# Kernel tuning notes

Hardware: AMD Instinct MI355X
Metric: run time of the kernel (lower is better)

The kernel has to match this reference:

```python
import jax, jax.numpy as jnp
import numpy as np

SR = 16000
WIN_LENGTH = int(round(SR / 1000.0 * 25))   # 400 samples
HOP_LENGTH = int(round(SR / 1000.0 * 10))   # 160 samples
EPSILON = 1e-12


def _hamming_window(n):
    # torch.hamming_window(n, periodic=True): 0.54 - 0.46*cos(2*pi*k/n)
    k = jnp.arange(n, dtype=jnp.float32)
    return 0.54 - 0.46 * jnp.cos(2.0 * jnp.pi * k / n)


def _fit_window(win, n_fft):
    # Replicates the module's pad-to / crop-to n_fft logic (static shapes).
    L = win.shape[0]
    if L < n_fft:
        pad = n_fft - L
        b = pad // 2
        win = jnp.concatenate([jnp.zeros(b, win.dtype), win, jnp.zeros(pad - b, win.dtype)])
    elif L > n_fft:
        c = (L - n_fft) // 2
        win = win[c:c + n_fft]
    return win


def setup_inputs() -> dict:
    key = jax.random.key(0)
    # (batch, time_step, n_fft//2 + 1, 2) real/imag onesided STFT
    x = jax.random.normal(key, (16, 3000, 201, 2), dtype=jnp.float32)
    return {"x": x}


def reference(x):
    B, T, F, _ = x.shape
    n_fft = 2 * (F - 1)                       # onesided=True
    xc = jax.lax.complex(x[..., 0], x[..., 1])
    # torch.irfft(..., normalized=False, onesided=True) == numpy-style irfft
    q = jnp.fft.irfft(xc, n=n_fft, axis=-1).astype(x.dtype)   # [B, T, n_fft]
    win = _fit_window(_hamming_window(WIN_LENGTH), n_fft)
    q = q * win
    est_len = (T - 1) * HOP_LENGTH + n_fft
    # Fused overlap-add via a single scatter-add instead of a per-frame loop.
    idx = jnp.arange(T)[:, None] * HOP_LENGTH + jnp.arange(n_fft)[None, :]  # [T, n_fft]
    istft = jnp.zeros((B, est_len), x.dtype).at[:, idx].add(q)
    sq_win = win * win
    ssw = jnp.zeros((est_len,), x.dtype).at[idx].add(jnp.broadcast_to(sq_win, (T, n_fft)))
    istft = jnp.where(ssw > EPSILON, istft / ssw, istft)
    # center=True: trim n_fft//2 on each side
    istft = istft[:, n_fft // 2: est_len - n_fft // 2]
    return istft
```

## Files before the change

### kernel.cpp

```cpp
#include <hip/hip_runtime.h>
#include <math.h>

constexpr int BB     = 16;
constexpr int T      = 3000;
constexpr int F      = 201;
constexpr int NFFT   = 400;
constexpr int HOP    = 160;
constexpr int K      = 402;
constexpr int KP     = 416;
constexpr int JP     = 480;
constexpr int ESTLEN = (T - 1) * HOP + NFFT;
constexpr int OUTLEN = ESTLEN - NFFT;
constexpr float EPS  = 1e-12f;

typedef short bf16x8 __attribute__((ext_vector_type(8)));
typedef float f32x4  __attribute__((ext_vector_type(4)));

__device__ __forceinline__ unsigned short f2bf(float f) {
    unsigned int u = __float_as_uint(f);
    u = (u + 0x7fffu + ((u >> 16) & 1u)) >> 16;
    return (unsigned short)u;
}


__global__ void build_wt2(unsigned short* __restrict__ Wt2) {
    int idx = blockIdx.x * blockDim.x + threadIdx.x;
    if (idx >= JP * KP) return;
    int j = idx / KP;
    int k = idx - j * KP;
    float v = 0.f;
    if (j < NFFT && k < K) {
        int f = k >> 1;
        bool is_re = (k & 1) == 0;
        float c = (f == 0 || f == F - 1) ? (1.f / 400.f) : (2.f / 400.f);
        int m = (j * f) % NFFT;
        float ang = (float)(2.0 * M_PI * (double)m / 400.0);
        float tw = is_re ? cosf(ang) : -sinf(ang);
        float win = 0.54f - 0.46f * cosf((float)(2.0 * M_PI * (double)j / 400.0));
        v = c * tw * win;
    }
    Wt2[idx] = f2bf(v);
}

__global__ void build_ssw(float* __restrict__ ssw) {
    int p = blockIdx.x * blockDim.x + threadIdx.x;
    if (p >= ESTLEN) return;
    int t_hi = p / HOP; if (t_hi > T - 1) t_hi = T - 1;
    int t_lo = (p >= NFFT) ? ((p - NFFT) / HOP + 1) : 0;
    float s = 0.f;
    for (int t = t_lo; t <= t_hi; ++t) {
        int j = p - t * HOP;
        float w = 0.54f - 0.46f * cosf((float)(2.0 * M_PI * (double)j / 400.0));
        s += w * w;
    }
    ssw[p] = s;
}


__global__ __launch_bounds__(256)
void istft_fused(const float* __restrict__ A, const unsigned short* __restrict__ Wt2,
                 const float* __restrict__ ssw, float* __restrict__ out) {
    __shared__ unsigned short As[66 * 40];
    __shared__ unsigned short Ws[JP * 32];

    const int tid  = threadIdx.x;
    const int lane = tid & 63;
    const int w    = tid >> 6;
    const int bx   = blockIdx.x;
    const int b    = blockIdx.y;
    const int u0   = 1 + bx * 64;

    const int lrow = lane & 15;
    const int lkg  = lane >> 4;

    f32x4 acc[10];
    #pragma unroll
    for (int mt = 0; mt < 10; ++mt) acc[mt] = (f32x4){0.f, 0.f, 0.f, 0.f};

    const int ar  = tid >> 2;
    const int akq = (tid & 3) * 8;

    for (int ks = 0; ks < 13; ++ks) {
        const int k0 = ks * 32;

        {
            #pragma unroll
            for (int pass = 0; pass < 2; ++pass) {
                int r  = (pass == 0) ? ar : (64 + (tid >> 2));
                bool active = (pass == 0) || (tid < 8);
                if (active) {
                    int t = u0 - 2 + r;
                    unsigned short vs[8];
                    if (t >= 0 && t < T) {
                        const float* src = A + ((size_t)(b * T + t)) * K + k0 + akq;
                        #pragma unroll
                        for (int i = 0; i < 4; ++i) {
                            int kk = k0 + akq + 2 * i;
                            float2 fv = make_float2(0.f, 0.f);
                            if (kk < K) fv = *reinterpret_cast<const float2*>(src + 2 * i);
                            vs[2 * i]     = f2bf(fv.x);
                            vs[2 * i + 1] = f2bf(fv.y);
                        }
                    } else {
                        #pragma unroll
                        for (int i = 0; i < 8; ++i) vs[i] = 0;
                    }
                    *reinterpret_cast<bf16x8*>(&As[r * 40 + akq]) =
                        *reinterpret_cast<const bf16x8*>(vs);
                }
            }
        }

        {
            #pragma unroll
            for (int it = 0; it < 8; ++it) {
                int P = it * 256 + tid;
                if (P < JP * 4) {
                    int j  = P >> 2;
                    int cp = P & 3;
                    int c  = cp ^ ((j >> 1) & 3);
                    const unsigned short* g = Wt2 + (size_t)j * KP + k0 + c * 8;
                    unsigned short* l = &Ws[(size_t)(it * 256 + w * 64) * 8];
                    __builtin_amdgcn_global_load_lds(
                        (const __attribute__((address_space(1))) void*)g,
                        (__attribute__((address_space(3))) void*)l,
                        16, 0, 0);
                }
            }
        }

        __syncthreads();

        bf16x8 afrag[3];
        #pragma unroll
        for (int dt = 0; dt < 3; ++dt) {
            int rs = w * 16 + lrow + 2 - dt;
            afrag[dt] = *reinterpret_cast<const bf16x8*>(&As[rs * 40 + lkg * 8]);
        }
        #pragma unroll
        for (int mt = 0; mt < 10; ++mt) {
            #pragma unroll
            for (int dt = 0; dt < 3; ++dt) {
                int j    = dt * 160 + mt * 16 + lrow;
                int phys = (j << 2) | (lkg ^ ((j >> 1) & 3));
                bf16x8 bfrag = *reinterpret_cast<const bf16x8*>(&Ws[phys * 8]);
                acc[mt] = __builtin_amdgcn_mfma_f32_16x16x32_bf16(
                    afrag[dt], bfrag, acc[mt], 0, 0, 0);
            }
        }

        __syncthreads();
    }

    #pragma unroll
    for (int mt = 0; mt < 10; ++mt) {
        int m = mt * 16 + lrow;
        #pragma unroll
        for (int q = 0; q < 4; ++q) {
            int u  = u0 + w * 16 + lkg * 4 + q;
            int pe = 160 * u + m;
            int po = pe - (NFFT / 2);
            if (po >= 0 && po < OUTLEN) {
                float s = ssw[pe];
                float v = acc[mt][q];
                out[(size_t)b * OUTLEN + po] = (s > EPS) ? v / s : v;
            }
        }
    }
}

extern "C" void kernel_launch(void* const* d_in, const int* in_sizes, int n_in,
                              void* d_out, int out_size, void* d_ws, size_t ws_size,
                              hipStream_t stream) {
    const float* x = (const float*)d_in[0];
    float* out = (float*)d_out;

    unsigned short* Wt2 = (unsigned short*)d_ws;
    float* ssw = (float*)((char*)d_ws + 400000);

    {
        int total = JP * KP;
        build_wt2<<<(total + 255) / 256, 256, 0, stream>>>(Wt2);
    }
    {
        build_ssw<<<(ESTLEN + 255) / 256, 256, 0, stream>>>(ssw);
    }
    {
        dim3 grid(47, BB);
        istft_fused<<<grid, 256, 0, stream>>>(x, Wt2, ssw, out);
    }
}
```

Measured before the change: 66.61 us.

## Double-buffer LDS staging and switch to 32x32 MFMA with larger frame tiles

Double-buffers the A and W tiles in shared memory so that global loads for the next K-slice overlap MFMA compute on the current one, with a single barrier per step. Moves from 16x16x32 to 32x32x16 bf16 MFMAs with 3 waves covering 96 frames per block (32x16 grid), which cuts redundant W staging per output. Precomputes reciprocal window-sum so the epilogue multiplies instead of divides. Shared memory roughly doubles and the 3-wave blocks with launch_bounds(192,2) change occupancy.

```diff
diff --git a/kernel.cpp b/kernel.cpp
--- a/kernel.cpp
+++ b/kernel.cpp
@@ -13,8 +13,15 @@
 constexpr int OUTLEN = ESTLEN - NFFT;
 constexpr float EPS  = 1e-12f;
 
+constexpr int UT      = 96;
+constexpr int AROWS   = 98;
+constexpr int ASTR    = 40;
+constexpr int NKS     = 13;
+constexpr int WS_HALF = JP * 32;
+constexpr int AS_HALF = AROWS * ASTR;
+
 typedef short bf16x8 __attribute__((ext_vector_type(8)));
-typedef float f32x4  __attribute__((ext_vector_type(4)));
+typedef float f32x16 __attribute__((ext_vector_type(16)));
 
 __device__ __forceinline__ unsigned short f2bf(float f) {
     unsigned int u = __float_as_uint(f);
@@ -42,7 +49,7 @@
     Wt2[idx] = f2bf(v);
 }
 
-__global__ void build_ssw(float* __restrict__ ssw) {
+__global__ void build_rssw(float* __restrict__ rssw) {
     int p = blockIdx.x * blockDim.x + threadIdx.x;
     if (p >= ESTLEN) return;
     int t_hi = p / HOP; if (t_hi > T - 1) t_hi = T - 1;
@@ -53,118 +60,167 @@
         float w = 0.54f - 0.46f * cosf((float)(2.0 * M_PI * (double)j / 400.0));
         s += w * w;
     }
-    ssw[p] = s;
-}
-
-
-__global__ __launch_bounds__(256)
+    rssw[p] = (s > EPS) ? 1.f / s : 1.f;
+}
+
+__global__ __launch_bounds__(192, 2)
 void istft_fused(const float* __restrict__ A, const unsigned short* __restrict__ Wt2,
-                 const float* __restrict__ ssw, float* __restrict__ out) {
-    __shared__ unsigned short As[66 * 40];
-    __shared__ unsigned short Ws[JP * 32];
+                 const float* __restrict__ rssw, float* __restrict__ out) {
+    __shared__ unsigned short Ws[2 * WS_HALF];
+    __shared__ unsigned short As[2 * AS_HALF];
 
     const int tid  = threadIdx.x;
     const int lane = tid & 63;
     const int w    = tid >> 6;
-    const int bx   = blockIdx.x;
+    const int lj   = lane & 31;
+    const int lh   = lane >> 5;
     const int b    = blockIdx.y;
-    const int u0   = 1 + bx * 64;
-
-    const int lrow = lane & 15;
-    const int lkg  = lane >> 4;
-
-    f32x4 acc[10];
+    const int u0   = 1 + blockIdx.x * UT;
+    const int tbase = u0 - 2;
+
+    f32x16 acc[5];
     #pragma unroll
-    for (int mt = 0; mt < 10; ++mt) acc[mt] = (f32x4){0.f, 0.f, 0.f, 0.f};
-
-    const int ar  = tid >> 2;
-    const int akq = (tid & 3) * 8;
-
-    for (int ks = 0; ks < 13; ++ks) {
-        const int k0 = ks * 32;
-
-        {
-            #pragma unroll
-            for (int pass = 0; pass < 2; ++pass) {
-                int r  = (pass == 0) ? ar : (64 + (tid >> 2));
-                bool active = (pass == 0) || (tid < 8);
-                if (active) {
-                    int t = u0 - 2 + r;
-                    unsigned short vs[8];
-                    if (t >= 0 && t < T) {
-                        const float* src = A + ((size_t)(b * T + t)) * K + k0 + akq;
-                        #pragma unroll
-                        for (int i = 0; i < 4; ++i) {
-                            int kk = k0 + akq + 2 * i;
-                            float2 fv = make_float2(0.f, 0.f);
-                            if (kk < K) fv = *reinterpret_cast<const float2*>(src + 2 * i);
-                            vs[2 * i]     = f2bf(fv.x);
-                            vs[2 * i + 1] = f2bf(fv.y);
-                        }
-                    } else {
-                        #pragma unroll
-                        for (int i = 0; i < 8; ++i) vs[i] = 0;
-                    }
-                    *reinterpret_cast<bf16x8*>(&As[r * 40 + akq]) =
-                        *reinterpret_cast<const bf16x8*>(vs);
+    for (int mt = 0; mt < 5; ++mt)
+        #pragma unroll
+        for (int i = 0; i < 16; ++i) acc[mt][i] = 0.f;
+
+    const int rm = tid >> 1;
+    const int hm = tid & 1;
+    const int tm = tbase + rm;
+    const bool vm = (tm >= 0 && tm < T);
+    const float* rowm = A + (size_t)(b * T + tm) * K;
+    const bool hasx = (tid < 8);
+    const int rx = 96 + (tid >> 2);
+    const int ox = tid & 3;
+    const int tx = tbase + rx;
+    const bool vx = hasx && (tx >= 0 && tx < T);
+    const float* rowx = A + (size_t)(b * T + tx) * K;
+
+    auto stage_W = [&](unsigned short* dst, int k0) {
+        #pragma unroll
+        for (int it = 0; it < 10; ++it) {
+            int P  = it * 192 + tid;
+            int j  = P >> 2;
+            int cp = P & 3;
+            int c  = cp ^ ((j >> 1) & 3);
+            const unsigned short* g = Wt2 + (size_t)j * KP + k0 + c * 8;
+            unsigned short* l = dst + (size_t)(it * 192 + w * 64) * 8;
+            __builtin_amdgcn_global_load_lds(
+                (const __attribute__((address_space(1))) void*)g,
+                (__attribute__((address_space(3))) void*)l, 16, 0, 0);
+        }
+    };
+
+    auto load_A = [&](int k0, float* a16, float* a8) {
+        int kb = k0 + hm * 16;
+        if (vm) {
+            if (kb + 16 <= K) {
+                #pragma unroll
+                for (int q = 0; q < 4; ++q)
+                    *reinterpret_cast<float4*>(&a16[q * 4]) =
+                        *reinterpret_cast<const float4*>(rowm + kb + q * 4);
+            } else {
+                #pragma unroll
+                for (int i = 0; i < 16; ++i)
+                    a16[i] = (kb + i < K) ? rowm[kb + i] : 0.f;
+            }
+        } else {
+            #pragma unroll
+            for (int i = 0; i < 16; ++i) a16[i] = 0.f;
+        }
+        int kx = k0 + ox * 8;
+        if (vx) {
+            if (kx + 8 <= K) {
+                #pragma unroll
+                for (int q = 0; q < 2; ++q)
+                    *reinterpret_cast<float4*>(&a8[q * 4]) =
+                        *reinterpret_cast<const float4*>(rowx + kx + q * 4);
+            } else {
+                #pragma unroll
+                for (int i = 0; i < 8; ++i)
+                    a8[i] = (kx + i < K) ? rowx[kx + i] : 0.f;
+            }
+        } else {
+            #pragma unroll
+            for (int i = 0; i < 8; ++i) a8[i] = 0.f;
+        }
+    };
+
+    auto write_A = [&](unsigned short* dst, const float* a16, const float* a8) {
+        unsigned short s[16];
+        #pragma unroll
+        for (int i = 0; i < 16; ++i) s[i] = f2bf(a16[i]);
+        *reinterpret_cast<bf16x8*>(&dst[rm * ASTR + hm * 16]) =
+            *reinterpret_cast<const bf16x8*>(&s[0]);
+        *reinterpret_cast<bf16x8*>(&dst[rm * ASTR + hm * 16 + 8]) =
+            *reinterpret_cast<const bf16x8*>(&s[8]);
+        if (hasx) {
+            unsigned short sx[8];
+            #pragma unroll
+            for (int i = 0; i < 8; ++i) sx[i] = f2bf(a8[i]);
+            *reinterpret_cast<bf16x8*>(&dst[rx * ASTR + ox * 8]) =
+                *reinterpret_cast<const bf16x8*>(&sx[0]);
+        }
+    };
+
+    auto compute = [&](const unsigned short* WsC, const unsigned short* AsC) {
+        bf16x8 af[3][2];
+        #pragma unroll
+        for (int dt = 0; dt < 3; ++dt)
+            #pragma unroll
+            for (int kh = 0; kh < 2; ++kh)
+                af[dt][kh] = *reinterpret_cast<const bf16x8*>(
+                    &AsC[(w * 32 + lj + 2 - dt) * ASTR + kh * 16 + lh * 8]);
+        #pragma unroll
+        for (int dt = 0; dt < 3; ++dt)
+            #pragma unroll
+            for (int kh = 0; kh < 2; ++kh)
+                #pragma unroll
+                for (int mt = 0; mt < 5; ++mt) {
+                    int j = dt * 160 + mt * 32 + lj;
+                    int c = (kh * 2 + lh) ^ ((lj >> 1) & 3);
+                    bf16x8 bf = *reinterpret_cast<const bf16x8*>(
+                        &WsC[(size_t)j * 32 + c * 8]);
+                    acc[mt] = __builtin_amdgcn_mfma_f32_32x32x16_bf16(
+                        af[dt][kh], bf, acc[mt], 0, 0, 0);
                 }
-            }
-        }
-
-        {
-            #pragma unroll
-            for (int it = 0; it < 8; ++it) {
-                int P = it * 256 + tid;
-                if (P < JP * 4) {
-                    int j  = P >> 2;
-                    int cp = P & 3;
-                    int c  = cp ^ ((j >> 1) & 3);
-                    const unsigned short* g = Wt2 + (size_t)j * KP + k0 + c * 8;
-                    unsigned short* l = &Ws[(size_t)(it * 256 + w * 64) * 8];
-                    __builtin_amdgcn_global_load_lds(
-                        (const __attribute__((address_space(1))) void*)g,
-                        (__attribute__((address_space(3))) void*)l,
-                        16, 0, 0);
-                }
-            }
-        }
-
+    };
+
+    {
+        float a16[16], a8[8];
+        load_A(0, a16, a8);
+        stage_W(&Ws[0], 0);
+        write_A(&As[0], a16, a8);
         __syncthreads();
-
-        bf16x8 afrag[3];
-        #pragma unroll
-        for (int dt = 0; dt < 3; ++dt) {
-            int rs = w * 16 + lrow + 2 - dt;
-            afrag[dt] = *reinterpret_cast<const bf16x8*>(&As[rs * 40 + lkg * 8]);
-        }
-        #pragma unroll
-        for (int mt = 0; mt < 10; ++mt) {
-            #pragma unroll
-            for (int dt = 0; dt < 3; ++dt) {
-                int j    = dt * 160 + mt * 16 + lrow;
-                int phys = (j << 2) | (lkg ^ ((j >> 1) & 3));
-                bf16x8 bfrag = *reinterpret_cast<const bf16x8*>(&Ws[phys * 8]);
-                acc[mt] = __builtin_amdgcn_mfma_f32_16x16x32_bf16(
-                    afrag[dt], bfrag, acc[mt], 0, 0, 0);
-            }
-        }
-
+    }
+
+    for (int ks = 0; ks < NKS; ++ks) {
+        unsigned short* WsC = &Ws[(ks & 1) * WS_HALF];
+        unsigned short* AsC = &As[(ks & 1) * AS_HALF];
+        unsigned short* WsN = &Ws[((ks & 1) ^ 1) * WS_HALF];
+        unsigned short* AsN = &As[((ks & 1) ^ 1) * AS_HALF];
+        float a16[16], a8[8];
+        const bool dn = (ks + 1 < NKS);
+        if (dn) {
+            load_A((ks + 1) * 32, a16, a8);
+            stage_W(WsN, (ks + 1) * 32);
+        }
+        compute(WsC, AsC);
+        if (dn) write_A(AsN, a16, a8);
         __syncthreads();
     }
 
     #pragma unroll
-    for (int mt = 0; mt < 10; ++mt) {
-        int m = mt * 16 + lrow;
-        #pragma unroll
-        for (int q = 0; q < 4; ++q) {
-            int u  = u0 + w * 16 + lkg * 4 + q;
-            int pe = 160 * u + m;
+    for (int mt = 0; mt < 5; ++mt) {
+        #pragma unroll
+        for (int rg = 0; rg < 16; ++rg) {
+            int urow = (rg & 3) + 8 * (rg >> 2) + 4 * lh;
+            int u  = u0 + w * 32 + urow;
+            int m  = mt * 32 + lj;
+            int pe = u * HOP + m;
             int po = pe - (NFFT / 2);
-            if (po >= 0 && po < OUTLEN) {
-                float s = ssw[pe];
-                float v = acc[mt][q];
-                out[(size_t)b * OUTLEN + po] = (s > EPS) ? v / s : v;
-            }
+            if (po >= 0 && po < OUTLEN)
+                out[(size_t)b * OUTLEN + po] = acc[mt][rg] * rssw[pe];
         }
     }
 }
@@ -176,17 +232,17 @@
     float* out = (float*)d_out;
 
     unsigned short* Wt2 = (unsigned short*)d_ws;
-    float* ssw = (float*)((char*)d_ws + 400000);
+    float* rssw = (float*)((char*)d_ws + 399360);
 
     {
         int total = JP * KP;
         build_wt2<<<(total + 255) / 256, 256, 0, stream>>>(Wt2);
     }
     {
-        build_ssw<<<(ESTLEN + 255) / 256, 256, 0, stream>>>(ssw);
-    }
-    {
-        dim3 grid(47, BB);
-        istft_fused<<<grid, 256, 0, stream>>>(x, Wt2, ssw, out);
-    }
-}
+        build_rssw<<<(ESTLEN + 255) / 256, 256, 0, stream>>>(rssw);
+    }
+    {
+        dim3 grid(32, BB);
+        istft_fused<<<grid, 192, 0, stream>>>(x, Wt2, rssw, out);
+    }
+}
```

New measurement: 74.61 us. 1.12x slower.

## Double-buffer LDS with async loads and enlarge per-block frame tile

Applied to the files above, without the earlier changes.

Restructures the fused iSTFT GEMM so each 512-thread block covers 192 frames instead of 64, cutting redundant halo loads and per-block weight traffic. The fp32 input and the basis weights are now streamed into double-buffered LDS with direct global-to-LDS loads, so the next K-slice arrives while MFMAs run on the current one. The bf16 conversion moves to fragment load time. The weights are pre-tiled per K-step, and the overlap-add normaliser is stored as a reciprocal so the epilogue multiplies instead of divides. In exchange it uses more LDS and registers, leaving fewer blocks per CU, and the grid drops to 256 blocks, which may underfill the GPU.

```diff
diff --git a/kernel.cpp b/kernel.cpp
--- a/kernel.cpp
+++ b/kernel.cpp
@@ -1,4 +1,5 @@
 #include <hip/hip_runtime.h>
+#include <hip/hip_bf16.h>
 #include <math.h>
 
 constexpr int BB     = 16;
@@ -7,11 +8,16 @@
 constexpr int NFFT   = 400;
 constexpr int HOP    = 160;
 constexpr int K      = 402;
-constexpr int KP     = 416;
-constexpr int JP     = 480;
 constexpr int ESTLEN = (T - 1) * HOP + NFFT;
 constexpr int OUTLEN = ESTLEN - NFFT;
 constexpr float EPS  = 1e-12f;
+
+constexpr int UT    = 192;
+constexpr int AR    = 194;
+constexpr int NSTEP = 13;
+constexpr int WJ    = 480;
+constexpr int WS_SH = WJ * 32;
+constexpr int AS_FL = AR * 32;
 
 typedef short bf16x8 __attribute__((ext_vector_type(8)));
 typedef float f32x4  __attribute__((ext_vector_type(4)));
@@ -22,12 +28,25 @@
     return (unsigned short)u;
 }
 
-
-__global__ void build_wt2(unsigned short* __restrict__ Wt2) {
+__device__ __forceinline__ bf16x8 cvt8(float4 a, float4 b) {
+    __hip_bfloat162 h0 = __float22bfloat162_rn(make_float2(a.x, a.y));
+    __hip_bfloat162 h1 = __float22bfloat162_rn(make_float2(a.z, a.w));
+    __hip_bfloat162 h2 = __float22bfloat162_rn(make_float2(b.x, b.y));
+    __hip_bfloat162 h3 = __float22bfloat162_rn(make_float2(b.z, b.w));
+    union U { bf16x8 v; __hip_bfloat162 h[4]; } u;
+    u.h[0] = h0; u.h[1] = h1; u.h[2] = h2; u.h[3] = h3;
+    return u.v;
+}
+
+
+__global__ void build_wt(unsigned short* __restrict__ Wg) {
     int idx = blockIdx.x * blockDim.x + threadIdx.x;
-    if (idx >= JP * KP) return;
-    int j = idx / KP;
-    int k = idx - j * KP;
+    if (idx >= NSTEP * WJ * 32) return;
+    int ksg = idx / (WJ * 32);
+    int rem = idx - ksg * (WJ * 32);
+    int j  = rem >> 5;
+    int kk = rem & 31;
+    int k  = ksg * 32 + kk;
     float v = 0.f;
     if (j < NFFT && k < K) {
         int f = k >> 1;
@@ -39,10 +58,10 @@
         float win = 0.54f - 0.46f * cosf((float)(2.0 * M_PI * (double)j / 400.0));
         v = c * tw * win;
     }
-    Wt2[idx] = f2bf(v);
-}
-
-__global__ void build_ssw(float* __restrict__ ssw) {
+    Wg[idx] = f2bf(v);
+}
+
+__global__ void build_rssw(float* __restrict__ rssw) {
     int p = blockIdx.x * blockDim.x + threadIdx.x;
     if (p >= ESTLEN) return;
     int t_hi = p / HOP; if (t_hi > T - 1) t_hi = T - 1;
@@ -53,120 +72,158 @@
         float w = 0.54f - 0.46f * cosf((float)(2.0 * M_PI * (double)j / 400.0));
         s += w * w;
     }
-    ssw[p] = s;
-}
-
-
-__global__ __launch_bounds__(256)
-void istft_fused(const float* __restrict__ A, const unsigned short* __restrict__ Wt2,
-                 const float* __restrict__ ssw, float* __restrict__ out) {
-    __shared__ unsigned short As[66 * 40];
-    __shared__ unsigned short Ws[JP * 32];
+    rssw[p] = (s > EPS) ? 1.f / s : 1.f;
+}
+
+__global__ __launch_bounds__(512)
+void istft_fused(const float* __restrict__ A, const unsigned short* __restrict__ Wg,
+                 const float* __restrict__ rssw, const float* __restrict__ zpage,
+                 float* __restrict__ out) {
+    __shared__ unsigned short Ws[2 * WS_SH];
+    __shared__ float As[2 * AS_FL + 16];
 
     const int tid  = threadIdx.x;
     const int lane = tid & 63;
     const int w    = tid >> 6;
-    const int bx   = blockIdx.x;
+    const int wu   = w >> 1;
+    const int wm   = w & 1;
+    const int l15  = lane & 15;
+    const int kg   = lane >> 4;
     const int b    = blockIdx.y;
-    const int u0   = 1 + bx * 64;
-
-    const int lrow = lane & 15;
-    const int lkg  = lane >> 4;
-
-    f32x4 acc[10];
-    #pragma unroll
-    for (int mt = 0; mt < 10; ++mt) acc[mt] = (f32x4){0.f, 0.f, 0.f, 0.f};
-
-    const int ar  = tid >> 2;
-    const int akq = (tid & 3) * 8;
-
-    for (int ks = 0; ks < 13; ++ks) {
-        const int k0 = ks * 32;
-
-        {
-            #pragma unroll
-            for (int pass = 0; pass < 2; ++pass) {
-                int r  = (pass == 0) ? ar : (64 + (tid >> 2));
-                bool active = (pass == 0) || (tid < 8);
-                if (active) {
-                    int t = u0 - 2 + r;
-                    unsigned short vs[8];
-                    if (t >= 0 && t < T) {
-                        const float* src = A + ((size_t)(b * T + t)) * K + k0 + akq;
-                        #pragma unroll
-                        for (int i = 0; i < 4; ++i) {
-                            int kk = k0 + akq + 2 * i;
-                            float2 fv = make_float2(0.f, 0.f);
-                            if (kk < K) fv = *reinterpret_cast<const float2*>(src + 2 * i);
-                            vs[2 * i]     = f2bf(fv.x);
-                            vs[2 * i + 1] = f2bf(fv.y);
-                        }
-                    } else {
-                        #pragma unroll
-                        for (int i = 0; i < 8; ++i) vs[i] = 0;
-                    }
-                    *reinterpret_cast<bf16x8*>(&As[r * 40 + akq]) =
-                        *reinterpret_cast<const bf16x8*>(vs);
+    const int u0   = 1 + blockIdx.x * UT;
+    const int tbase = u0 - 2;
+
+    f32x4 acc[3][5];
+    #pragma unroll
+    for (int i = 0; i < 3; ++i)
+        #pragma unroll
+        for (int mf = 0; mf < 5; ++mf)
+            #pragma unroll
+            for (int q = 0; q < 4; ++q) acc[i][mf][q] = 0.f;
+
+    const float* a_src[13];
+    #pragma unroll
+    for (int p = 0; p < 13; ++p) {
+        int P  = p * 512 + tid;
+        int r  = P >> 5;
+        int pd = P & 31;
+        int ld = pd ^ ((r & 6) << 2);
+        int t  = tbase + r;
+        bool v = (P < AR * 32) && (t >= 0 && t < T);
+        a_src[p] = v ? (A + (size_t)(b * T + t) * K + ld) : (zpage + ld);
+    }
+    const unsigned short* w_src[4];
+    #pragma unroll
+    for (int p = 0; p < 4; ++p) w_src[p] = Wg + (size_t)(p * 512 + tid) * 8;
+
+    auto issue_W = [&](int buf, int ksg) {
+        unsigned short* dstb = &Ws[buf * WS_SH];
+        #pragma unroll
+        for (int p = 0; p < 4; ++p) {
+            int P = p * 512 + tid;
+            if (P < WJ * 4) {
+                __builtin_amdgcn_global_load_lds(
+                    (const __attribute__((address_space(1))) void*)(w_src[p] + (size_t)ksg * WS_SH),
+                    (__attribute__((address_space(3))) void*)(dstb + (p * 512 + w * 64) * 8),
+                    16, 0, 0);
+            }
+        }
+    };
+
+    auto issue_A = [&](int buf, int k0) {
+        float* dstb = &As[buf * AS_FL];
+        #pragma unroll
+        for (int p = 0; p < 13; ++p) {
+            int P = p * 512 + tid;
+            if (P < AR * 32) {
+                __builtin_amdgcn_global_load_lds(
+                    (const __attribute__((address_space(1))) void*)(a_src[p] + k0),
+                    (__attribute__((address_space(3))) void*)(dstb + p * 512 + w * 64),
+                    4, 0, 0);
+            }
+        }
+    };
+
+    auto stage_A0 = [&]() {
+        #pragma unroll
+        for (int p = 0; p < 4; ++p) {
+            int C = p * 512 + tid;
+            if (C < AR * 8) {
+                int r  = C >> 3;
+                int cp = C & 7;
+                int cl = cp ^ (r & 6);
+                int k  = 384 + cl * 4;
+                int t  = tbase + r;
+                float4 v = make_float4(0.f, 0.f, 0.f, 0.f);
+                if (t >= 0 && t < T) {
+                    const float* sr = A + (size_t)(b * T + t) * K;
+                    v.x = (k + 0 < K) ? sr[k + 0] : 0.f;
+                    v.y = (k + 1 < K) ? sr[k + 1] : 0.f;
+                    v.z = (k + 2 < K) ? sr[k + 2] : 0.f;
+                    v.w = (k + 3 < K) ? sr[k + 3] : 0.f;
                 }
-            }
-        }
-
-        {
-            #pragma unroll
-            for (int it = 0; it < 8; ++it) {
-                int P = it * 256 + tid;
-                if (P < JP * 4) {
-                    int j  = P >> 2;
-                    int cp = P & 3;
-                    int c  = cp ^ ((j >> 1) & 3);
-                    const unsigned short* g = Wt2 + (size_t)j * KP + k0 + c * 8;
-                    unsigned short* l = &Ws[(size_t)(it * 256 + w * 64) * 8];
-                    __builtin_amdgcn_global_load_lds(
-                        (const __attribute__((address_space(1))) void*)g,
-                        (__attribute__((address_space(3))) void*)l,
-                        16, 0, 0);
-                }
-            }
-        }
-
+                *reinterpret_cast<float4*>(&As[C * 4]) = v;
+            }
+        }
+    };
+
+    auto compute = [&](int buf) {
+        const float* Ab = &As[buf * AS_FL];
+        const unsigned short* Wb = &Ws[buf * WS_SH];
+        bf16x8 af[3][3];
+        #pragma unroll
+        for (int i = 0; i < 3; ++i)
+            #pragma unroll
+            for (int dt = 0; dt < 3; ++dt) {
+                int r  = wu * 48 + 16 * i + l15 + (2 - dt);
+                int s0 = (2 * kg) ^ (r & 6);
+                float4 lo = *reinterpret_cast<const float4*>(&Ab[r * 32 + s0 * 4]);
+                float4 hi = *reinterpret_cast<const float4*>(&Ab[r * 32 + (s0 ^ 1) * 4]);
+                af[i][dt] = cvt8(lo, hi);
+            }
+        #pragma unroll
+        for (int dt = 0; dt < 3; ++dt) {
+            bf16x8 bf[5];
+            #pragma unroll
+            for (int mf = 0; mf < 5; ++mf) {
+                int j = dt * 160 + wm * 80 + mf * 16 + l15;
+                bf[mf] = *reinterpret_cast<const bf16x8*>(&Wb[j * 32 + kg * 8]);
+            }
+            #pragma unroll
+            for (int i = 0; i < 3; ++i)
+                #pragma unroll
+                for (int mf = 0; mf < 5; ++mf)
+                    acc[i][mf] = __builtin_amdgcn_mfma_f32_16x16x32_bf16(
+                        af[i][dt], bf[mf], acc[i][mf], 0, 0, 0);
+        }
+    };
+
+    stage_A0();
+    issue_W(0, 12);
+    __syncthreads();
+
+    for (int s = 0; s < NSTEP; ++s) {
+        if (s + 1 < NSTEP) {
+            issue_W((s + 1) & 1, s);
+            issue_A((s + 1) & 1, s * 32);
+        }
+        compute(s & 1);
         __syncthreads();
-
-        bf16x8 afrag[3];
-        #pragma unroll
-        for (int dt = 0; dt < 3; ++dt) {
-            int rs = w * 16 + lrow + 2 - dt;
-            afrag[dt] = *reinterpret_cast<const bf16x8*>(&As[rs * 40 + lkg * 8]);
-        }
-        #pragma unroll
-        for (int mt = 0; mt < 10; ++mt) {
-            #pragma unroll
-            for (int dt = 0; dt < 3; ++dt) {
-                int j    = dt * 160 + mt * 16 + lrow;
-                int phys = (j << 2) | (lkg ^ ((j >> 1) & 3));
-                bf16x8 bfrag = *reinterpret_cast<const bf16x8*>(&Ws[phys * 8]);
-                acc[mt] = __builtin_amdgcn_mfma_f32_16x16x32_bf16(
-                    afrag[dt], bfrag, acc[mt], 0, 0, 0);
-            }
-        }
-
-        __syncthreads();
-    }
-
-    #pragma unroll
-    for (int mt = 0; mt < 10; ++mt) {
-        int m = mt * 16 + lrow;
-        #pragma unroll
-        for (int q = 0; q < 4; ++q) {
-            int u  = u0 + w * 16 + lkg * 4 + q;
-            int pe = 160 * u + m;
-            int po = pe - (NFFT / 2);
-            if (po >= 0 && po < OUTLEN) {
-                float s = ssw[pe];
-                float v = acc[mt][q];
-                out[(size_t)b * OUTLEN + po] = (s > EPS) ? v / s : v;
-            }
-        }
-    }
+    }
+
+    #pragma unroll
+    for (int i = 0; i < 3; ++i)
+        #pragma unroll
+        for (int mf = 0; mf < 5; ++mf)
+            #pragma unroll
+            for (int q = 0; q < 4; ++q) {
+                int u  = u0 + wu * 48 + 16 * i + kg * 4 + q;
+                int m  = wm * 80 + mf * 16 + l15;
+                int pe = u * HOP + m;
+                int po = pe - (NFFT / 2);
+                if (po >= 0 && po < OUTLEN)
+                    out[(size_t)b * OUTLEN + po] = acc[i][mf][q] * rssw[pe];
+            }
 }
 
 extern "C" void kernel_launch(void* const* d_in, const int* in_sizes, int n_in,
@@ -175,18 +232,21 @@
     const float* x = (const float*)d_in[0];
     float* out = (float*)d_out;
 
-    unsigned short* Wt2 = (unsigned short*)d_ws;
-    float* ssw = (float*)((char*)d_ws + 400000);
-
+    char* ws = (char*)d_ws;
+    unsigned short* Wg = (unsigned short*)ws;
+    float* rssw = (float*)(ws + 399360);
+    float* zpage = (float*)(ws + 399360 + 1920960);
+
+    hipMemsetAsync(zpage, 0, 2048, stream);
     {
-        int total = JP * KP;
-        build_wt2<<<(total + 255) / 256, 256, 0, stream>>>(Wt2);
+        int total = NSTEP * WJ * 32;
+        build_wt<<<(total + 255) / 256, 256, 0, stream>>>(Wg);
     }
     {
-        build_ssw<<<(ESTLEN + 255) / 256, 256, 0, stream>>>(ssw);
+        build_rssw<<<(ESTLEN + 255) / 256, 256, 0, stream>>>(rssw);
     }
     {
-        dim3 grid(47, BB);
-        istft_fused<<<grid, 256, 0, stream>>>(x, Wt2, ssw, out);
-    }
-}
+        dim3 grid(16, BB);
+        istft_fused<<<grid, 512, 0, stream>>>(x, Wg, rssw, zpage, out);
+    }
+}
```

Result: slower. 96.77 us (+45.3%).
